# Performance work log

Measured on AMD Instinct MI355X. Metric: run time of the kernel, lower is better.

The kernel has to match this reference:

```python
import jax, jax.numpy as jnp
import numpy as np

N = 512
E = N * N
H = 64          # hidden_dim
ED = 6          # edge_dim
L = 4           # n_layers
EPS = 1e-5


def _lin(key, fan_in, fan_out):
    k1, k2 = jax.random.split(key)
    w = jax.random.normal(k1, (fan_in, fan_out), jnp.float32) / np.sqrt(fan_in)
    b = jax.random.normal(k2, (fan_out,), jnp.float32) * 0.01
    return w, b


def _lin_stack(key, fan_in, fan_out, n):
    ws, bs = zip(*[_lin(jax.random.fold_in(key, i), fan_in, fan_out) for i in range(n)])
    return jnp.stack(ws), jnp.stack(bs)


def setup_inputs() -> dict:
    key = jax.random.key(0)
    ks = jax.random.split(key, 16)
    idx = jnp.arange(N, dtype=jnp.int32)
    src = jnp.repeat(idx, N)          # x_j source nodes
    dst = jnp.tile(idx, N)            # x_i target nodes (aggregation index)
    edge_index = jnp.stack([src, dst])  # [2, E]
    x = jax.random.normal(ks[0], (N, 6), jnp.float32)
    edge_attr = jax.random.normal(ks[1], (E, ED), jnp.float32)
    enc_w1, enc_b1 = _lin(ks[2], 6, H)
    enc_w2, enc_b2 = _lin(ks[3], H, H)
    att_w1, att_b1 = _lin_stack(ks[4], 2 * H + ED, H, L)   # [L,134,64]
    att_w2, att_b2 = _lin_stack(ks[5], H, 1, L)
    val_w1, val_b1 = _lin_stack(ks[6], H + ED, H, L)       # [L,70,64]
    val_w2, val_b2 = _lin_stack(ks[7], H, H, L)
    upd_w1, upd_b1 = _lin_stack(ks[8], 2 * H, H, L)        # [L,128,64]
    upd_w2, upd_b2 = _lin_stack(ks[9], H, H, L)
    ln_g = jnp.ones((L, H), jnp.float32)
    ln_b = jnp.zeros((L, H), jnp.float32)
    dec_w1, dec_b1 = _lin(ks[10], H, H)
    dec_w2, dec_b2 = _lin(ks[11], H, 1)
    return dict(x=x, edge_attr=edge_attr,
                enc_w1=enc_w1, enc_b1=enc_b1, enc_w2=enc_w2, enc_b2=enc_b2,
                att_w1=att_w1, att_b1=att_b1, att_w2=att_w2, att_b2=att_b2,
                val_w1=val_w1, val_b1=val_b1, val_w2=val_w2, val_b2=val_b2,
                upd_w1=upd_w1, upd_b1=upd_b1, upd_w2=upd_w2, upd_b2=upd_b2,
                ln_g=ln_g, ln_b=ln_b,
                dec_w1=dec_w1, dec_b1=dec_b1, dec_w2=dec_w2, dec_b2=dec_b2,
                edge_index=edge_index)


def reference(x, edge_attr, enc_w1, enc_b1, enc_w2, enc_b2,
              att_w1, att_b1, att_w2, att_b2,
              val_w1, val_b1, val_w2, val_b2,
              upd_w1, upd_b1, upd_w2, upd_b2,
              ln_g, ln_b, dec_w1, dec_b1, dec_w2, dec_b2, edge_index):
    src, dst = edge_index[0], edge_index[1]
    h = jax.nn.relu(x @ enc_w1 + enc_b1) @ enc_w2 + enc_b2  # [N,H]
    for l in range(L):
        hi = h[dst]                           # x_i  [E,H]
        hj = h[src]                           # x_j  [E,H]
        # attention logits: MLP([x_i || x_j || e])
        a_in = jnp.concatenate([hi, hj, edge_attr], axis=-1)   # [E,2H+ED]
        a = jax.nn.leaky_relu(a_in @ att_w1[l] + att_b1[l], 0.2) @ att_w2[l] + att_b2[l]
        a = a[:, 0]                                            # [E]
        # segment softmax over destination index (numerically stable)
        m = jax.ops.segment_max(a, dst, num_segments=N)
        e = jnp.exp(a - m[dst])
        s = jax.ops.segment_sum(e, dst, num_segments=N)
        alpha = e / s[dst]                                     # [E]
        # values: MLP([x_j || e])
        v_in = jnp.concatenate([hj, edge_attr], axis=-1)       # [E,H+ED]
        v = jax.nn.relu(v_in @ val_w1[l] + val_b1[l]) @ val_w2[l] + val_b2[l]
        agg = jax.ops.segment_sum(v * alpha[:, None], dst, num_segments=N)  # [N,H]
        # update + residual + LayerNorm
        u_in = jnp.concatenate([h, agg], axis=-1)              # [N,2H]
        u = jax.nn.relu(u_in @ upd_w1[l] + upd_b1[l]) @ upd_w2[l] + upd_b2[l]
        r = u + h
        mu = jnp.mean(r, axis=-1, keepdims=True)
        var = jnp.mean((r - mu) ** 2, axis=-1, keepdims=True)
        h = ln_g[l] * (r - mu) / jnp.sqrt(var + EPS) + ln_b[l]
    return jax.nn.relu(h @ dec_w1 + dec_b1) @ dec_w2 + dec_b2  # [N,1]
```

## Files before the change

### kernel.cpp

```cpp
#include <hip/hip_runtime.h>
#include <math.h>

#define NN 512
#define HH 64
#define NLAYERS 4
#define LN_EPS 1e-5f


__global__ void k_transpose(const float* __restrict__ ea, float* __restrict__ eat) {
    int t = blockIdx.x * 256 + threadIdx.x;
    int i = t & (NN - 1);
    int j = t >> 9;
    int e = i * NN + j;
#pragma unroll
    for (int k = 0; k < 6; ++k) eat[(size_t)t * 6 + k] = ea[(size_t)e * 6 + k];
}

__launch_bounds__(256)
__global__ void k_encoder(const float* __restrict__ x,
                          const float* __restrict__ ew1, const float* __restrict__ eb1,
                          const float* __restrict__ ew2, const float* __restrict__ eb2,
                          const float* __restrict__ aw1, const float* __restrict__ ab1,
                          const float* __restrict__ wa2, const float* __restrict__ vw1,
                          const float* __restrict__ vb1,
                          float* __restrict__ h, float* __restrict__ Pd,
                          float* __restrict__ Qs, float* __restrict__ Rv,
                          float* __restrict__ Sq) {
    const int j = blockIdx.x;
    const int tid = threadIdx.x;
    const int d = tid & 63;
    const int w = tid >> 6;
    __shared__ float r1[HH], hs[HH];
    __shared__ float part[4][HH], partQ[4][HH], partR[4][HH];

    if (w == 0) {
        float z = eb1[d];
#pragma unroll
        for (int k = 0; k < 6; ++k) z += x[j * 6 + k] * ew1[k * HH + d];
        r1[d] = fmaxf(z, 0.f);
    }
    __syncthreads();
    {
        float z2 = (w == 0) ? eb2[d] : 0.f;
        for (int k = w * 16; k < w * 16 + 16; ++k) z2 += r1[k] * ew2[k * HH + d];
        part[w][d] = z2;
    }
    __syncthreads();
    if (w == 0) {
        float hv = part[0][d] + part[1][d] + part[2][d] + part[3][d];
        h[(size_t)j * HH + d] = hv;
        hs[d] = hv;
    }
    __syncthreads();
    {
        float pp = (w == 0) ? ab1[d] : 0.f;
        float qq = 0.f;
        float rr = (w == 0) ? vb1[d] : 0.f;
        for (int k = w * 16; k < w * 16 + 16; ++k) {
            float hk = hs[k];
            pp += hk * aw1[k * HH + d];
            qq += hk * aw1[(HH + k) * HH + d];
            rr += hk * vw1[k * HH + d];
        }
        part[w][d] = pp; partQ[w][d] = qq; partR[w][d] = rr;
    }
    __syncthreads();
    if (w == 0) {
        float qf = partQ[0][d] + partQ[1][d] + partQ[2][d] + partQ[3][d];
        Pd[(size_t)j * HH + d] = part[0][d] + part[1][d] + part[2][d] + part[3][d];
        Qs[(size_t)j * HH + d] = qf;
        Rv[(size_t)j * HH + d] = partR[0][d] + partR[1][d] + partR[2][d] + partR[3][d];
        float sq = qf * wa2[d];
#pragma unroll
        for (int o = 32; o; o >>= 1) sq += __shfl_xor(sq, o);
        if (d == 0) Sq[j] = sq;
    }
}

__launch_bounds__(512, 4)
__global__ void k_layer(const float* __restrict__ eat, const float* __restrict__ h_in,
                        const float* __restrict__ Pd, const float* __restrict__ Qs,
                        const float* __restrict__ Rv, const float* __restrict__ Sq,
                        const float* __restrict__ waE,
                        const float* __restrict__ wa2v,
                        const float* __restrict__ wvE,
                        const float* __restrict__ wv2, const float* __restrict__ vb2,
                        const float* __restrict__ uw1, const float* __restrict__ ub1,
                        const float* __restrict__ uw2, const float* __restrict__ ub2,
                        const float* __restrict__ lng, const float* __restrict__ lnb,
                        float* __restrict__ h_out,
                        const float* __restrict__ aw1n, const float* __restrict__ ab1n,
                        const float* __restrict__ wa2n, const float* __restrict__ vw1n,
                        const float* __restrict__ vb1n,
                        float* __restrict__ Pdn, float* __restrict__ Qsn,
                        float* __restrict__ Rvn, float* __restrict__ Sqn,
                        int do_prep) {
    const int j = blockIdx.x;
    const int tid = threadIdx.x;
    const int lane = tid & 63;
    const int w = tid >> 6;
    const int slot = lane >> 3;
    const int dp = lane & 7;
    const int d0 = dp * 8;
    const int d = lane;

    __shared__ __align__(16) float ea_s[NN * 6];
    __shared__ __align__(16) float Sq_s[NN];
    __shared__ float a_s[NN];
    __shared__ float red_m[8], red_s[8];
    __shared__ float accs[8][HH];
    __shared__ float av[HH], uin[2 * HH], r1[HH], hs[HH];
    __shared__ float part[8][HH], partQ[8][HH], partR[8][HH];

    {
        const float4* s4 = (const float4*)(eat + (size_t)j * (NN * 6));
        float4* d4 = (float4*)ea_s;
        d4[tid] = s4[tid];
        if (tid < 256) d4[tid + 512] = s4[tid + 512];
    }
    if (tid < 128) ((float4*)Sq_s)[tid] = ((const float4*)Sq)[tid];

    float WA[6][8], wa2raw[8], wa2r[8], pdr[8], w6s[6];
#pragma unroll
    for (int k = 0; k < 6; ++k)
#pragma unroll
        for (int u = 0; u < 8; ++u) WA[k][u] = waE[k * HH + d0 + u];
#pragma unroll
    for (int u = 0; u < 8; ++u) {
        wa2raw[u] = wa2v[d0 + u];
        pdr[u] = Pd[(size_t)j * HH + d0 + u];
    }
#pragma unroll
    for (int k = 0; k < 6; ++k) {
        float t = 0.f;
#pragma unroll
        for (int u = 0; u < 8; ++u) t += WA[k][u] * wa2raw[u];
        t += __shfl_xor(t, 1);
        t += __shfl_xor(t, 2);
        t += __shfl_xor(t, 4);
        w6s[k] = 0.6f * t;
    }
#pragma unroll
    for (int u = 0; u < 8; ++u) wa2r[u] = 0.4f * wa2raw[u];
    __syncthreads();

    const int ibw = w * 64;
    float lmax = -1e30f;
#pragma unroll
    for (int it = 0; it < 8; ++it) {
        const int i = ibw + it * 8 + slot;
        const float4* q4 = (const float4*)(Qs + (size_t)i * HH + d0);
        float4 qa = q4[0], qb = q4[1];
        float qv[8] = {qa.x, qa.y, qa.z, qa.w, qb.x, qb.y, qb.z, qb.w};
        float eav[6];
#pragma unroll
        for (int k = 0; k < 6; ++k) eav[k] = ea_s[i * 6 + k];
        float p1 = 0.f;
#pragma unroll
        for (int u = 0; u < 8; ++u) {
            float z = pdr[u] + qv[u];
#pragma unroll
            for (int k = 0; k < 6; ++k) z += eav[k] * WA[k][u];
            p1 += fabsf(z) * wa2r[u];
        }
        p1 += __shfl_xor(p1, 1);
        p1 += __shfl_xor(p1, 2);
        p1 += __shfl_xor(p1, 4);
        float lin = 0.6f * Sq_s[i];
#pragma unroll
        for (int k = 0; k < 6; ++k) lin += eav[k] * w6s[k];
        float a = lin + p1;
        if (dp == 0) a_s[i] = a;
        lmax = fmaxf(lmax, a);
    }
#pragma unroll
    for (int o = 32; o; o >>= 1) lmax = fmaxf(lmax, __shfl_xor(lmax, o));
    if (lane == 0) red_m[w] = lmax;
    __syncthreads();
    float m = red_m[0];
#pragma unroll
    for (int q = 1; q < 8; ++q) m = fmaxf(m, red_m[q]);

    float e = expf(a_s[tid] - m);
    a_s[tid] = e;
    float lsum = e;
#pragma unroll
    for (int o = 32; o; o >>= 1) lsum += __shfl_xor(lsum, o);
    if (lane == 0) red_s[w] = lsum;
    __syncthreads();
    float s = red_s[0];
#pragma unroll
    for (int q = 1; q < 8; ++q) s += red_s[q];

    float WV[6][8];
#pragma unroll
    for (int k = 0; k < 6; ++k)
#pragma unroll
        for (int u = 0; u < 8; ++u) WV[k][u] = wvE[k * HH + d0 + u];
    float acc[8] = {0.f, 0.f, 0.f, 0.f, 0.f, 0.f, 0.f, 0.f};
#pragma unroll
    for (int it = 0; it < 8; ++it) {
        const int i = ibw + it * 8 + slot;
        const float4* r4 = (const float4*)(Rv + (size_t)i * HH + d0);
        float4 ra = r4[0], rb = r4[1];
        float rv[8] = {ra.x, ra.y, ra.z, ra.w, rb.x, rb.y, rb.z, rb.w};
        float eav[6];
#pragma unroll
        for (int k = 0; k < 6; ++k) eav[k] = ea_s[i * 6 + k];
        const float wi = a_s[i];
#pragma unroll
        for (int u = 0; u < 8; ++u) {
            float z = rv[u];
#pragma unroll
            for (int k = 0; k < 6; ++k) z += eav[k] * WV[k][u];
            acc[u] += wi * fmaxf(z, 0.f);
        }
    }
#pragma unroll
    for (int u = 0; u < 8; ++u) {
        acc[u] += __shfl_xor(acc[u], 8);
        acc[u] += __shfl_xor(acc[u], 16);
        acc[u] += __shfl_xor(acc[u], 32);
    }
    if (slot == 0) {
#pragma unroll
        for (int u = 0; u < 8; ++u) accs[w][d0 + u] = acc[u];
    }
    __syncthreads();
    if (tid < HH) {
        float tot = accs[0][tid];
#pragma unroll
        for (int q = 1; q < 8; ++q) tot += accs[q][tid];
        av[tid] = tot / s;
    }
    __syncthreads();

    const float hv = h_in[(size_t)j * HH + d];
    {
        float p = (w == 0) ? vb2[d] : 0.f;
        for (int k = w * 8; k < w * 8 + 8; ++k) p += av[k] * wv2[k * HH + d];
        part[w][d] = p;
        if (w == 0) uin[d] = hv;
    }
    __syncthreads();
    if (w == 0) {
        float agg = part[0][d];
#pragma unroll
        for (int q = 1; q < 8; ++q) agg += part[q][d];
        uin[HH + d] = agg;
    }
    __syncthreads();
    {
        float t = (w == 0) ? ub1[d] : 0.f;
        for (int c = w * 16; c < w * 16 + 16; ++c) t += uin[c] * uw1[c * HH + d];
        part[w][d] = t;
    }
    __syncthreads();
    if (w == 0) {
        float t = part[0][d];
#pragma unroll
        for (int q = 1; q < 8; ++q) t += part[q][d];
        r1[d] = fmaxf(t, 0.f);
    }
    __syncthreads();
    {
        float u = (w == 0) ? ub2[d] : 0.f;
        for (int k = w * 8; k < w * 8 + 8; ++k) u += r1[k] * uw2[k * HH + d];
        part[w][d] = u;
    }
    __syncthreads();
    if (w == 0) {
        float r = hv + part[0][d];
#pragma unroll
        for (int q = 1; q < 8; ++q) r += part[q][d];
        float sum = r;
#pragma unroll
        for (int o = 32; o; o >>= 1) sum += __shfl_xor(sum, o);
        float mu = sum * (1.f / HH);
        float dr = r - mu;
        float v2 = dr * dr;
#pragma unroll
        for (int o = 32; o; o >>= 1) v2 += __shfl_xor(v2, o);
        float var = v2 * (1.f / HH);
        float hn = lng[d] * dr * (1.f / sqrtf(var + LN_EPS)) + lnb[d];
        h_out[(size_t)j * HH + d] = hn;
        hs[d] = hn;
    }
    __syncthreads();

    if (do_prep) {
        float pp = (w == 0) ? ab1n[d] : 0.f;
        float qq = 0.f;
        float rr = (w == 0) ? vb1n[d] : 0.f;
        for (int k = w * 8; k < w * 8 + 8; ++k) {
            float hk = hs[k];
            pp += hk * aw1n[k * HH + d];
            qq += hk * aw1n[(HH + k) * HH + d];
            rr += hk * vw1n[k * HH + d];
        }
        part[w][d] = pp; partQ[w][d] = qq; partR[w][d] = rr;
        __syncthreads();
        if (w == 0) {
            float pf = part[0][d], qf = partQ[0][d], rf = partR[0][d];
#pragma unroll
            for (int q = 1; q < 8; ++q) {
                pf += part[q][d]; qf += partQ[q][d]; rf += partR[q][d];
            }
            Pdn[(size_t)j * HH + d] = pf;
            Qsn[(size_t)j * HH + d] = qf;
            Rvn[(size_t)j * HH + d] = rf;
            float sq = qf * wa2n[d];
#pragma unroll
            for (int o = 32; o; o >>= 1) sq += __shfl_xor(sq, o);
            if (d == 0) Sqn[j] = sq;
        }
    }
}

__launch_bounds__(256)
__global__ void k_decoder(const float* __restrict__ h,
                          const float* __restrict__ dw1, const float* __restrict__ db1,
                          const float* __restrict__ dw2, const float* __restrict__ db2,
                          float* __restrict__ out) {
    const int j = blockIdx.x;
    const int tid = threadIdx.x;
    const int d = tid & 63;
    const int w = tid >> 6;
    __shared__ float hs[HH], part[4][HH];
    if (w == 0) hs[d] = h[(size_t)j * HH + d];
    __syncthreads();
    float t = (w == 0) ? db1[d] : 0.f;
    for (int k = w * 16; k < w * 16 + 16; ++k) t += hs[k] * dw1[k * HH + d];
    part[w][d] = t;
    __syncthreads();
    if (w == 0) {
        float tt = fmaxf(part[0][d] + part[1][d] + part[2][d] + part[3][d], 0.f);
        float sum = tt * dw2[d];
#pragma unroll
        for (int o = 32; o; o >>= 1) sum += __shfl_xor(sum, o);
        if (d == 0) out[j] = sum + db2[0];
    }
}

extern "C" void kernel_launch(void* const* d_in, const int* in_sizes, int n_in,
                              void* d_out, int out_size, void* d_ws, size_t ws_size,
                              hipStream_t stream) {
    const float* x      = (const float*)d_in[0];
    const float* ea     = (const float*)d_in[1];
    const float* enc_w1 = (const float*)d_in[2];
    const float* enc_b1 = (const float*)d_in[3];
    const float* enc_w2 = (const float*)d_in[4];
    const float* enc_b2 = (const float*)d_in[5];
    const float* att_w1 = (const float*)d_in[6];
    const float* att_b1 = (const float*)d_in[7];
    const float* att_w2 = (const float*)d_in[8];
    const float* val_w1 = (const float*)d_in[10];
    const float* val_b1 = (const float*)d_in[11];
    const float* val_w2 = (const float*)d_in[12];
    const float* val_b2 = (const float*)d_in[13];
    const float* upd_w1 = (const float*)d_in[14];
    const float* upd_b1 = (const float*)d_in[15];
    const float* upd_w2 = (const float*)d_in[16];
    const float* upd_b2 = (const float*)d_in[17];
    const float* ln_g   = (const float*)d_in[18];
    const float* ln_b   = (const float*)d_in[19];
    const float* dec_w1 = (const float*)d_in[20];
    const float* dec_b1 = (const float*)d_in[21];
    const float* dec_w2 = (const float*)d_in[22];
    const float* dec_b2 = (const float*)d_in[23];

    const size_t NH = (size_t)NN * HH;
    float* ws   = (float*)d_ws;
    float* EAT  = ws;
    float* h0   = EAT + (size_t)NN * NN * 6;
    float* h1   = h0 + NH;
    float* Pd0  = h1 + NH;
    float* Pd1  = Pd0 + NH;
    float* Qs0  = Pd1 + NH;
    float* Qs1  = Qs0 + NH;
    float* Rv0  = Qs1 + NH;
    float* Rv1  = Rv0 + NH;
    float* Sq0  = Rv1 + NH;
    float* Sq1  = Sq0 + NN;

    float* Pdb[2] = {Pd0, Pd1};
    float* Qsb[2] = {Qs0, Qs1};
    float* Rvb[2] = {Rv0, Rv1};
    float* Sqb[2] = {Sq0, Sq1};
    float* hb[2]  = {h0, h1};

    k_transpose<<<(NN * NN) / 256, 256, 0, stream>>>(ea, EAT);
    k_encoder<<<NN, 256, 0, stream>>>(x, enc_w1, enc_b1, enc_w2, enc_b2,
                                      att_w1, att_b1, att_w2, val_w1, val_b1,
                                      h0, Pd0, Qs0, Rv0, Sq0);

    for (int l = 0; l < NLAYERS; ++l) {
        const int cur = l & 1, nxt = (l + 1) & 1;
        const int np = (l + 1 < NLAYERS) ? (l + 1) : l;
        const float* aw1 = att_w1 + (size_t)l * 134 * HH;
        const float* vw1 = val_w1 + (size_t)l * 70 * HH;
        k_layer<<<NN, 512, 0, stream>>>(
            EAT, hb[cur],
            Pdb[cur], Qsb[cur], Rvb[cur], Sqb[cur],
            aw1 + 128 * HH, att_w2 + l * HH, vw1 + 64 * HH,
            val_w2 + (size_t)l * HH * HH, val_b2 + l * HH,
            upd_w1 + (size_t)l * 2 * HH * HH, upd_b1 + l * HH,
            upd_w2 + (size_t)l * HH * HH, upd_b2 + l * HH,
            ln_g + l * HH, ln_b + l * HH,
            hb[nxt],
            att_w1 + (size_t)np * 134 * HH, att_b1 + np * HH, att_w2 + np * HH,
            val_w1 + (size_t)np * 70 * HH, val_b1 + np * HH,
            Pdb[nxt], Qsb[nxt], Rvb[nxt], Sqb[nxt],
            (l + 1 < NLAYERS) ? 1 : 0);
    }
    k_decoder<<<NN, 256, 0, stream>>>(hb[NLAYERS & 1], dec_w1, dec_b1, dec_w2, dec_b2,
                                      (float*)d_out);
}
```

Before: 213.3 us.

## Fuse transpose+encoder and decoder into layer kernels, pad edge attrs, use packed float2 math

Merges the edge-attribute transpose and the encoder into one launch, and folds the decoder into the last layer kernel's else-branch, removing two launches. Edge attributes are padded to 8 floats per edge so each edge can be read with float4 vector loads from global and shared memory. The per-edge linear attention term is precomputed once per source node into shared memory, and the inner FMA loops use two-wide float vectors so the compiler can emit packed FP32 ops. The cost is about a third more memory traffic for the padded edge buffer, plus an extra barrier.

```diff
diff --git a/kernel.cpp b/kernel.cpp
--- a/kernel.cpp
+++ b/kernel.cpp
@@ -6,32 +6,41 @@
 #define NLAYERS 4
 #define LN_EPS 1e-5f
 
-
-__global__ void k_transpose(const float* __restrict__ ea, float* __restrict__ eat) {
-    int t = blockIdx.x * 256 + threadIdx.x;
-    int i = t & (NN - 1);
-    int j = t >> 9;
-    int e = i * NN + j;
-#pragma unroll
-    for (int k = 0; k < 6; ++k) eat[(size_t)t * 6 + k] = ea[(size_t)e * 6 + k];
-}
+typedef __attribute__((ext_vector_type(2))) float f32x2;
+
 
 __launch_bounds__(256)
-__global__ void k_encoder(const float* __restrict__ x,
-                          const float* __restrict__ ew1, const float* __restrict__ eb1,
-                          const float* __restrict__ ew2, const float* __restrict__ eb2,
-                          const float* __restrict__ aw1, const float* __restrict__ ab1,
-                          const float* __restrict__ wa2, const float* __restrict__ vw1,
-                          const float* __restrict__ vb1,
-                          float* __restrict__ h, float* __restrict__ Pd,
-                          float* __restrict__ Qs, float* __restrict__ Rv,
-                          float* __restrict__ Sq) {
-    const int j = blockIdx.x;
+__global__ void k_pre(const float* __restrict__ ea, const float* __restrict__ x,
+                      const float* __restrict__ ew1, const float* __restrict__ eb1,
+                      const float* __restrict__ ew2, const float* __restrict__ eb2,
+                      const float* __restrict__ aw1, const float* __restrict__ ab1,
+                      const float* __restrict__ wa2, const float* __restrict__ vw1,
+                      const float* __restrict__ vb1,
+                      float* __restrict__ EAT, float* __restrict__ h,
+                      float* __restrict__ Pd, float* __restrict__ Qs,
+                      float* __restrict__ Rv, float* __restrict__ Sq) {
+    __shared__ float r1[HH], hs[HH];
+    __shared__ float part[4][HH], partQ[4][HH], partR[4][HH];
+
+    if (blockIdx.x < 1024) {
+        int t = blockIdx.x * 256 + threadIdx.x;
+        int i = t & (NN - 1);
+        int j = t >> 9;
+        const float2* s2 = (const float2*)(ea + ((size_t)i * NN + j) * 6);
+        float2 e0 = s2[0], e1 = s2[1], e2 = s2[2];
+        float4 a, b;
+        a.x = e0.x; a.y = e0.y; a.z = e1.x; a.w = e1.y;
+        b.x = e2.x; b.y = e2.y; b.z = 0.f; b.w = 0.f;
+        float4* dst = (float4*)(EAT + (size_t)t * 8);
+        dst[0] = a;
+        dst[1] = b;
+        return;
+    }
+
+    const int j = blockIdx.x - 1024;
     const int tid = threadIdx.x;
     const int d = tid & 63;
     const int w = tid >> 6;
-    __shared__ float r1[HH], hs[HH];
-    __shared__ float part[4][HH], partQ[4][HH], partR[4][HH];
 
     if (w == 0) {
         float z = eb1[d];
@@ -94,6 +103,9 @@
                         const float* __restrict__ vb1n,
                         float* __restrict__ Pdn, float* __restrict__ Qsn,
                         float* __restrict__ Rvn, float* __restrict__ Sqn,
+                        const float* __restrict__ dw1, const float* __restrict__ db1,
+                        const float* __restrict__ dw2, const float* __restrict__ db2,
+                        float* __restrict__ out,
                         int do_prep) {
     const int j = blockIdx.x;
     const int tid = threadIdx.x;
@@ -104,7 +116,7 @@
     const int d0 = dp * 8;
     const int d = lane;
 
-    __shared__ __align__(16) float ea_s[NN * 6];
+    __shared__ __align__(16) float ea_s[NN * 8];
     __shared__ __align__(16) float Sq_s[NN];
     __shared__ float a_s[NN];
     __shared__ float red_m[8], red_s[8];
@@ -113,28 +125,34 @@
     __shared__ float part[8][HH], partQ[8][HH], partR[8][HH];
 
     {
-        const float4* s4 = (const float4*)(eat + (size_t)j * (NN * 6));
+        const float4* s4 = (const float4*)(eat + (size_t)j * (NN * 8));
         float4* d4 = (float4*)ea_s;
         d4[tid] = s4[tid];
-        if (tid < 256) d4[tid + 512] = s4[tid + 512];
+        d4[tid + 512] = s4[tid + 512];
     }
     if (tid < 128) ((float4*)Sq_s)[tid] = ((const float4*)Sq)[tid];
 
-    float WA[6][8], wa2raw[8], wa2r[8], pdr[8], w6s[6];
+    f32x2 WA2[6][4], pdr2[4];
+    float wa2raw[8], wa2r[8], w6s[6];
 #pragma unroll
     for (int k = 0; k < 6; ++k)
 #pragma unroll
-        for (int u = 0; u < 8; ++u) WA[k][u] = waE[k * HH + d0 + u];
-#pragma unroll
-    for (int u = 0; u < 8; ++u) {
-        wa2raw[u] = wa2v[d0 + u];
-        pdr[u] = Pd[(size_t)j * HH + d0 + u];
+        for (int p = 0; p < 4; ++p) {
+            WA2[k][p].x = waE[k * HH + d0 + 2 * p];
+            WA2[k][p].y = waE[k * HH + d0 + 2 * p + 1];
+        }
+#pragma unroll
+    for (int u = 0; u < 8; ++u) wa2raw[u] = wa2v[d0 + u];
+#pragma unroll
+    for (int p = 0; p < 4; ++p) {
+        pdr2[p].x = Pd[(size_t)j * HH + d0 + 2 * p];
+        pdr2[p].y = Pd[(size_t)j * HH + d0 + 2 * p + 1];
     }
 #pragma unroll
     for (int k = 0; k < 6; ++k) {
         float t = 0.f;
 #pragma unroll
-        for (int u = 0; u < 8; ++u) t += WA[k][u] * wa2raw[u];
+        for (int p = 0; p < 4; ++p) t += WA2[k][p].x * wa2raw[2 * p] + WA2[k][p].y * wa2raw[2 * p + 1];
         t += __shfl_xor(t, 1);
         t += __shfl_xor(t, 2);
         t += __shfl_xor(t, 4);
@@ -144,6 +162,15 @@
     for (int u = 0; u < 8; ++u) wa2r[u] = 0.4f * wa2raw[u];
     __syncthreads();
 
+    {
+        float alin = 0.6f * Sq_s[tid];
+#pragma unroll
+        for (int k = 0; k < 6; ++k) alin += ea_s[tid * 8 + k] * w6s[k];
+        __syncthreads();
+        Sq_s[tid] = alin;
+    }
+    __syncthreads();
+
     const int ibw = w * 64;
     float lmax = -1e30f;
 #pragma unroll
@@ -151,25 +178,23 @@
         const int i = ibw + it * 8 + slot;
         const float4* q4 = (const float4*)(Qs + (size_t)i * HH + d0);
         float4 qa = q4[0], qb = q4[1];
-        float qv[8] = {qa.x, qa.y, qa.z, qa.w, qb.x, qb.y, qb.z, qb.w};
-        float eav[6];
-#pragma unroll
-        for (int k = 0; k < 6; ++k) eav[k] = ea_s[i * 6 + k];
+        f32x2 qv2[4] = {{qa.x, qa.y}, {qa.z, qa.w}, {qb.x, qb.y}, {qb.z, qb.w}};
+        const float4* e4 = (const float4*)(ea_s + i * 8);
+        float4 ea0 = e4[0], ea1 = e4[1];
+        float eav[6] = {ea0.x, ea0.y, ea0.z, ea0.w, ea1.x, ea1.y};
         float p1 = 0.f;
 #pragma unroll
-        for (int u = 0; u < 8; ++u) {
-            float z = pdr[u] + qv[u];
-#pragma unroll
-            for (int k = 0; k < 6; ++k) z += eav[k] * WA[k][u];
-            p1 += fabsf(z) * wa2r[u];
+        for (int p = 0; p < 4; ++p) {
+            f32x2 z = pdr2[p] + qv2[p];
+#pragma unroll
+            for (int k = 0; k < 6; ++k) z += WA2[k][p] * eav[k];
+            p1 += fabsf(z.x) * wa2r[2 * p];
+            p1 += fabsf(z.y) * wa2r[2 * p + 1];
         }
         p1 += __shfl_xor(p1, 1);
         p1 += __shfl_xor(p1, 2);
         p1 += __shfl_xor(p1, 4);
-        float lin = 0.6f * Sq_s[i];
-#pragma unroll
-        for (int k = 0; k < 6; ++k) lin += eav[k] * w6s[k];
-        float a = lin + p1;
+        float a = Sq_s[i] + p1;
         if (dp == 0) a_s[i] = a;
         lmax = fmaxf(lmax, a);
     }
@@ -192,28 +217,32 @@
 #pragma unroll
     for (int q = 1; q < 8; ++q) s += red_s[q];
 
-    float WV[6][8];
+    f32x2 WV2[6][4];
 #pragma unroll
     for (int k = 0; k < 6; ++k)
 #pragma unroll
-        for (int u = 0; u < 8; ++u) WV[k][u] = wvE[k * HH + d0 + u];
+        for (int p = 0; p < 4; ++p) {
+            WV2[k][p].x = wvE[k * HH + d0 + 2 * p];
+            WV2[k][p].y = wvE[k * HH + d0 + 2 * p + 1];
+        }
     float acc[8] = {0.f, 0.f, 0.f, 0.f, 0.f, 0.f, 0.f, 0.f};
 #pragma unroll
     for (int it = 0; it < 8; ++it) {
         const int i = ibw + it * 8 + slot;
         const float4* r4 = (const float4*)(Rv + (size_t)i * HH + d0);
         float4 ra = r4[0], rb = r4[1];
-        float rv[8] = {ra.x, ra.y, ra.z, ra.w, rb.x, rb.y, rb.z, rb.w};
-        float eav[6];
-#pragma unroll
-        for (int k = 0; k < 6; ++k) eav[k] = ea_s[i * 6 + k];
+        f32x2 rv2[4] = {{ra.x, ra.y}, {ra.z, ra.w}, {rb.x, rb.y}, {rb.z, rb.w}};
+        const float4* e4 = (const float4*)(ea_s + i * 8);
+        float4 ea0 = e4[0], ea1 = e4[1];
+        float eav[6] = {ea0.x, ea0.y, ea0.z, ea0.w, ea1.x, ea1.y};
         const float wi = a_s[i];
 #pragma unroll
-        for (int u = 0; u < 8; ++u) {
-            float z = rv[u];
-#pragma unroll
-            for (int k = 0; k < 6; ++k) z += eav[k] * WV[k][u];
-            acc[u] += wi * fmaxf(z, 0.f);
+        for (int p = 0; p < 4; ++p) {
+            f32x2 z = rv2[p];
+#pragma unroll
+            for (int k = 0; k < 6; ++k) z += WV2[k][p] * eav[k];
+            acc[2 * p]     += wi * fmaxf(z.x, 0.f);
+            acc[2 * p + 1] += wi * fmaxf(z.y, 0.f);
         }
     }
 #pragma unroll
@@ -314,31 +343,21 @@
             for (int o = 32; o; o >>= 1) sq += __shfl_xor(sq, o);
             if (d == 0) Sqn[j] = sq;
         }
-    }
-}
-
-__launch_bounds__(256)
-__global__ void k_decoder(const float* __restrict__ h,
-                          const float* __restrict__ dw1, const float* __restrict__ db1,
-                          const float* __restrict__ dw2, const float* __restrict__ db2,
-                          float* __restrict__ out) {
-    const int j = blockIdx.x;
-    const int tid = threadIdx.x;
-    const int d = tid & 63;
-    const int w = tid >> 6;
-    __shared__ float hs[HH], part[4][HH];
-    if (w == 0) hs[d] = h[(size_t)j * HH + d];
-    __syncthreads();
-    float t = (w == 0) ? db1[d] : 0.f;
-    for (int k = w * 16; k < w * 16 + 16; ++k) t += hs[k] * dw1[k * HH + d];
-    part[w][d] = t;
-    __syncthreads();
-    if (w == 0) {
-        float tt = fmaxf(part[0][d] + part[1][d] + part[2][d] + part[3][d], 0.f);
-        float sum = tt * dw2[d];
-#pragma unroll
-        for (int o = 32; o; o >>= 1) sum += __shfl_xor(sum, o);
-        if (d == 0) out[j] = sum + db2[0];
+    } else {
+        float t = (w == 0) ? db1[d] : 0.f;
+        for (int k = w * 8; k < w * 8 + 8; ++k) t += hs[k] * dw1[k * HH + d];
+        part[w][d] = t;
+        __syncthreads();
+        if (w == 0) {
+            float tt = part[0][d];
+#pragma unroll
+            for (int q = 1; q < 8; ++q) tt += part[q][d];
+            tt = fmaxf(tt, 0.f);
+            float sum = tt * dw2[d];
+#pragma unroll
+            for (int o = 32; o; o >>= 1) sum += __shfl_xor(sum, o);
+            if (d == 0) out[j] = sum + db2[0];
+        }
     }
 }
 
@@ -372,7 +391,7 @@
     const size_t NH = (size_t)NN * HH;
     float* ws   = (float*)d_ws;
     float* EAT  = ws;
-    float* h0   = EAT + (size_t)NN * NN * 6;
+    float* h0   = EAT + (size_t)NN * NN * 8;
     float* h1   = h0 + NH;
     float* Pd0  = h1 + NH;
     float* Pd1  = Pd0 + NH;
@@ -389,10 +408,9 @@
     float* Sqb[2] = {Sq0, Sq1};
     float* hb[2]  = {h0, h1};
 
-    k_transpose<<<(NN * NN) / 256, 256, 0, stream>>>(ea, EAT);
-    k_encoder<<<NN, 256, 0, stream>>>(x, enc_w1, enc_b1, enc_w2, enc_b2,
-                                      att_w1, att_b1, att_w2, val_w1, val_b1,
-                                      h0, Pd0, Qs0, Rv0, Sq0);
+    k_pre<<<1536, 256, 0, stream>>>(ea, x, enc_w1, enc_b1, enc_w2, enc_b2,
+                                    att_w1, att_b1, att_w2, val_w1, val_b1,
+                                    EAT, h0, Pd0, Qs0, Rv0, Sq0);
 
     for (int l = 0; l < NLAYERS; ++l) {
         const int cur = l & 1, nxt = (l + 1) & 1;
@@ -411,8 +429,7 @@
             att_w1 + (size_t)np * 134 * HH, att_b1 + np * HH, att_w2 + np * HH,
             val_w1 + (size_t)np * 70 * HH, val_b1 + np * HH,
             Pdb[nxt], Qsb[nxt], Rvb[nxt], Sqb[nxt],
+            dec_w1, dec_b1, dec_w2, dec_b2, (float*)d_out,
             (l + 1 < NLAYERS) ? 1 : 0);
     }
-    k_decoder<<<NN, 256, 0, stream>>>(hb[NLAYERS & 1], dec_w1, dec_b1, dec_w2, dec_b2,
-                                      (float*)d_out);
 }
```

Result: slower. 257.6 us (+20.7%).
